# Performance work log

Hardware: AMD Instinct MI355X
Metric: run time of the kernel (lower is better)

## Reference

```python
import jax, jax.numpy as jnp
import numpy as np

N = 200000   # nodes
E = 3200000  # edges
G = 8192     # graphs
F_IN = 28    # one-hot node feature dim (dataset.num_node_features)
D = 50       # embed_dim
H = 16       # hidden_channels
C = 2        # num_classes


def setup_inputs() -> dict:
    key = jax.random.key(0)
    ks = jax.random.split(key, 12)
    x = jax.random.normal(ks[0], (N, F_IN), jnp.float32)
    row = jax.random.randint(ks[1], (E,), 0, N)   # source nodes (edge_index[0])
    col = jax.random.randint(ks[2], (E,), 0, N)   # target nodes (edge_index[1])
    edge_attr = jax.random.uniform(ks[3], (E,), jnp.float32)
    batch = jnp.sort(jax.random.randint(ks[4], (N,), 0, G))
    emb = jax.random.normal(ks[5], (F_IN, D), jnp.float32) * 0.1
    W1 = jax.random.normal(ks[6], (D, H), jnp.float32) * (1.0 / np.sqrt(D))
    b1 = jnp.zeros((H,), jnp.float32)
    W2 = jax.random.normal(ks[7], (H, H), jnp.float32) * (1.0 / np.sqrt(H))
    b2 = jnp.zeros((H,), jnp.float32)
    W3 = jax.random.normal(ks[8], (H, C), jnp.float32) * (1.0 / np.sqrt(H))
    b3 = jnp.zeros((C,), jnp.float32)
    return dict(x=x, row=row, col=col, edge_attr=edge_attr, batch=batch,
                emb=emb, W1=W1, b1=b1, W2=W2, b2=b2, W3=W3, b3=b3)


def gcn_conv(h, row, col, ew, W, b):
    """PyG GCNConv with normalize=True, add_self_loops=True (fill_value=1)."""
    # degree at target nodes, including self-loop weight 1
    deg = jax.ops.segment_sum(ew, col, num_segments=N) + 1.0
    dinv = jnp.where(deg > 0, deg ** -0.5, 0.0)
    hw = h @ W                                   # [N, out]
    norm = dinv[row] * ew * dinv[col]            # [E]
    agg = jax.ops.segment_sum(hw[row] * norm[:, None], col, num_segments=N)
    agg = agg + hw * (dinv * dinv)[:, None]      # self-loop contribution
    return agg + b


def reference(x, row, col, edge_attr, batch, emb, W1, b1, W2, b2, W3, b3):
    # x is one-hot-ish -> argmax -> embedding lookup
    h = emb[jnp.argmax(x, axis=1)]               # [N, D]
    h = jax.nn.relu(gcn_conv(h, row, col, edge_attr, W1, b1))
    # dropout is identity in eval mode
    h = jax.nn.relu(gcn_conv(h, row, col, edge_attr, W2, b2))
    h = gcn_conv(h, row, col, edge_attr, W3, b3)  # [N, C]
    # global mean pool over graphs
    sums = jax.ops.segment_sum(h, batch, num_segments=G)
    cnts = jax.ops.segment_sum(jnp.ones((N,), h.dtype), batch, num_segments=G)
    pooled = sums / jnp.maximum(cnts, 1.0)[:, None]  # [G, C]
    return jax.nn.softmax(pooled, axis=1)
```

## Files before the change

kernel.cpp:

```cpp
#include <hip/hip_runtime.h>
#include <hip/hip_fp16.h>

constexpr int Nn  = 200000;
constexpr int Ne  = 3200000;
constexpr int Ng  = 8192;
constexpr int FIN = 28;
constexpr int DE  = 50;
constexpr int HD  = 16;
constexpr int CD  = 2;

constexpr int NBIN   = (Nn + 255) >> 8;
constexpr int NBLK   = 256;
constexpr int CH     = (Ne + NBLK - 1) / NBLK;
constexpr int CSTR   = 800;
constexpr int LDSCAP = 4608;

__device__ __forceinline__ float dec_ea(unsigned u) {
  return ((float)(u & 16383u) + 0.5f) * (1.0f / 16384.0f);
}

static inline int nblocks(long long n, int bs = 256, int cap = 16384) {
  long long b = (n + bs - 1) / bs;
  return (int)(b < cap ? b : cap);
}

__global__ void k_zero(float* __restrict__ p, int n) {
  int i = blockIdx.x * blockDim.x + threadIdx.x;
  if (i < n) p[i] = 0.0f;
}

__global__ __launch_bounds__(256) void k_count(const int* __restrict__ col,
                                               int* __restrict__ counts) {
  __shared__ int c[NBIN];
  for (int i = threadIdx.x; i < NBIN; i += 256) c[i] = 0;
  __syncthreads();
  int lo = blockIdx.x * CH, hi = min(lo + CH, Ne);
  for (int e = lo + threadIdx.x; e < hi; e += 256) atomicAdd(&c[col[e] >> 8], 1);
  __syncthreads();
  for (int i = threadIdx.x; i < NBIN; i += 256) counts[blockIdx.x * CSTR + i] = c[i];
}

__global__ __launch_bounds__(256) void k_scan1b(int* __restrict__ counts,
                                                int* __restrict__ colTotal) {
  __shared__ int s[256];
  int bin = blockIdx.x, t = threadIdx.x;
  int v = counts[t * CSTR + bin];
  s[t] = v;
  __syncthreads();
  for (int d = 1; d < 256; d <<= 1) {
    int x = (t >= d) ? s[t - d] : 0;
    __syncthreads();
    s[t] += x;
    __syncthreads();
  }
  counts[t * CSTR + bin] = s[t] - v;
  if (t == 255) colTotal[bin] = s[t];
}

__global__ __launch_bounds__(1024) void k_scanBins(const int* __restrict__ colTotal,
                                                   int* __restrict__ binBase,
                                                   int* __restrict__ start) {
  __shared__ int s[1024];
  int t = threadIdx.x;
  int v = (t < NBIN) ? colTotal[t] : 0;
  s[t] = v;
  __syncthreads();
  for (int d = 1; d < 1024; d <<= 1) {
    int x = (t >= d) ? s[t - d] : 0;
    __syncthreads();
    s[t] += x;
    __syncthreads();
  }
  if (t < NBIN) binBase[t] = s[t] - v;
  if (t == NBIN - 1) { binBase[NBIN] = s[t]; start[Nn] = s[t]; }
}

__global__ __launch_bounds__(256) void k_place(const int* __restrict__ row,
                                               const int* __restrict__ col,
                                               const float* __restrict__ ea,
                                               const int* __restrict__ counts,
                                               const int* __restrict__ binBase,
                                               unsigned long long* __restrict__ staged) {
  __shared__ int base[NBIN];
  __shared__ int cur[NBIN];
  for (int i = threadIdx.x; i < NBIN; i += 256) {
    base[i] = binBase[i] + counts[blockIdx.x * CSTR + i];
    cur[i] = 0;
  }
  __syncthreads();
  int lo = blockIdx.x * CH, hi = min(lo + CH, Ne);
  for (int e = lo + threadIdx.x; e < hi; e += 256) {
    int c = col[e], bin = c >> 8;
    unsigned q = (unsigned)__float2int_rd(ea[e] * 16384.0f);
    if (q > 16383u) q = 16383u;
    unsigned lo32 = ((unsigned)row[e] << 14) | q;
    int off = atomicAdd(&cur[bin], 1);
    staged[base[bin] + off] = ((unsigned long long)(unsigned)c << 32) | lo32;
  }
}

__global__ __launch_bounds__(256) void k_fine(const int* __restrict__ binBase,
                                              const unsigned long long* __restrict__ staged,
                                              unsigned* __restrict__ csr,
                                              int* __restrict__ start,
                                              float* __restrict__ dinv) {
  __shared__ int ncnt[256];
  __shared__ int noff[256];
  __shared__ int ncur[256];
  __shared__ float sdeg[256];
  __shared__ unsigned outb[LDSCAP];
  int b = blockIdx.x, t = threadIdx.x;
  int lo = binBase[b];
  int cnt = binBase[b + 1] - lo;
  if (cnt > LDSCAP) cnt = LDSCAP;
  ncnt[t] = 0; ncur[t] = 0; sdeg[t] = 0.0f;
  __syncthreads();
  for (int i = t; i < cnt; i += 256) {
    unsigned long long p = staged[lo + i];
    int cl = (int)((p >> 32) & 255u);
    atomicAdd(&ncnt[cl], 1);
    atomicAdd(&sdeg[cl], dec_ea((unsigned)p));
  }
  __syncthreads();
  int v = ncnt[t];
  noff[t] = v;
  __syncthreads();
  for (int d = 1; d < 256; d <<= 1) {
    int x = (t >= d) ? noff[t - d] : 0;
    __syncthreads();
    noff[t] += x;
    __syncthreads();
  }
  int excl = noff[t] - v;
  __syncthreads();
  noff[t] = excl;
  __syncthreads();
  for (int i = t; i < cnt; i += 256) {
    unsigned long long p = staged[lo + i];
    int cl = (int)((p >> 32) & 255u);
    int idx = noff[cl] + atomicAdd(&ncur[cl], 1);
    outb[idx] = (unsigned)p;
  }
  __syncthreads();
  for (int i = t; i < cnt; i += 256) csr[lo + i] = outb[i];
  int node = (b << 8) + t;
  if (node < Nn) {
    start[node] = lo + noff[t];
    dinv[node] = rsqrtf(sdeg[t] + 1.0f);
  }
}

__global__ void k_embw(const float* __restrict__ emb, const float* __restrict__ W1,
                       float* __restrict__ EW1) {
  int t = threadIdx.x;
  if (t < FIN * HD) {
    int i = t / HD, k = t % HD;
    float s = 0.0f;
    for (int j = 0; j < DE; ++j) s += emb[i * DE + j] * W1[j * HD + k];
    EW1[t] = s;
  }
}

__global__ void k_embed(const float* __restrict__ x, const float* __restrict__ EW1,
                        const float* __restrict__ dinv, __half* __restrict__ hws, int n) {
  int stride = gridDim.x * blockDim.x;
  for (int i = blockIdx.x * blockDim.x + threadIdx.x; i < n; i += stride) {
    const float* xp = x + (long long)i * FIN;
    int arg = 0; float best = xp[0];
#pragma unroll
    for (int j = 1; j < FIN; ++j) { float v = xp[j]; if (v > best) { best = v; arg = j; } }
    float di = dinv[i];
    const float* ep = EW1 + arg * HD;
#pragma unroll
    for (int k = 0; k < HD; ++k) hws[((size_t)i << 4) + k] = __float2half(ep[k] * di);
  }
}

template <int OUTC>
__global__ __launch_bounds__(256) void k_conv(const int* __restrict__ start,
                                              const unsigned* __restrict__ csr,
                                              const __half* __restrict__ hws,
                                              const float* __restrict__ dinv,
                                              const float* __restrict__ bias,
                                              const float* __restrict__ Wn,
                                              __half* __restrict__ outw) {
  int n = blockIdx.x * 4 + (threadIdx.x >> 6);
  if (n >= Nn) return;
  int lane = threadIdx.x & 63;
  int slot = lane >> 3;
  int p    = lane & 7;
  const __half2* h2 = (const __half2*)hws;
  int lo = start[n], hi = start[n + 1];
  float ax = 0.0f, ay = 0.0f;
  for (int j = lo + slot; j < hi; j += 8) {
    unsigned u = csr[j];
    int r = u >> 14;
    float w = dec_ea(u);
    float2 v = __half22float2(h2[(r << 3) + p]);
    ax = fmaf(v.x, w, ax);
    ay = fmaf(v.y, w, ay);
  }
#pragma unroll
  for (int d = 8; d < 64; d <<= 1) {
    ax += __shfl_xor(ax, d, 64);
    ay += __shfl_xor(ay, d, 64);
  }
  float di = dinv[n];
  float2 self = __half22float2(h2[(n << 3) + p]);
  float h0 = fmaxf(di * (ax + self.x) + bias[2 * p + 0], 0.0f);
  float h1 = fmaxf(di * (ay + self.y) + bias[2 * p + 1], 0.0f);
  int k = lane & 15;
  float acc2 = 0.0f;
#pragma unroll
  for (int q = 0; q < 8; ++q) {
    float hj0 = __shfl(h0, q, 64);
    float hj1 = __shfl(h1, q, 64);
    acc2 = fmaf(hj0, Wn[(2 * q + 0) * OUTC + (OUTC == 16 ? k : (k & 1))], acc2);
    acc2 = fmaf(hj1, Wn[(2 * q + 1) * OUTC + (OUTC == 16 ? k : (k & 1))], acc2);
  }
  acc2 *= di;
  if (OUTC == 16) {
    if (lane < 16) outw[((size_t)n << 4) + k] = __float2half(acc2);
  } else {
    if (lane < CD) outw[(size_t)n * CD + k] = __float2half(acc2);
  }
}

__global__ __launch_bounds__(256) void k_conv3pool(const int* __restrict__ start,
                                                   const unsigned* __restrict__ csr,
                                                   const __half* __restrict__ h3,
                                                   const float* __restrict__ dinv,
                                                   const float* __restrict__ b3,
                                                   const int* __restrict__ batch,
                                                   float* __restrict__ sums,
                                                   float* __restrict__ cnts) {
  int wid = threadIdx.x >> 6;
  int lane = threadIdx.x & 63;
  int nsub = lane >> 2;
  int slot = lane & 3;
  int n = (blockIdx.x * 4 + wid) * 16 + nsub;
  if (n >= Nn) return;
  const __half2* h2 = (const __half2*)h3;
  int lo = start[n], hi = start[n + 1];
  float ax = 0.0f, ay = 0.0f;
  for (int j = lo + slot; j < hi; j += 4) {
    unsigned u = csr[j];
    int r = u >> 14;
    float w = dec_ea(u);
    float2 v = __half22float2(h2[r]);
    ax = fmaf(v.x, w, ax);
    ay = fmaf(v.y, w, ay);
  }
  ax += __shfl_xor(ax, 1, 64); ay += __shfl_xor(ay, 1, 64);
  ax += __shfl_xor(ax, 2, 64); ay += __shfl_xor(ay, 2, 64);
  if (slot == 0) {
    float di = dinv[n];
    float2 self = __half22float2(h2[n]);
    float a0 = di * (ax + self.x) + b3[0];
    float a1 = di * (ay + self.y) + b3[1];
    int g = batch[n];
    atomicAdd(&sums[2 * g + 0], a0);
    atomicAdd(&sums[2 * g + 1], a1);
    atomicAdd(&cnts[g], 1.0f);
  }
}

__global__ void k_softmax(const float* __restrict__ sums, const float* __restrict__ cnts,
                          float* __restrict__ out, int g) {
  int stride = gridDim.x * blockDim.x;
  for (int i = blockIdx.x * blockDim.x + threadIdx.x; i < g; i += stride) {
    float cnt = fmaxf(cnts[i], 1.0f);
    float c0 = sums[i * 2 + 0] / cnt;
    float c1 = sums[i * 2 + 1] / cnt;
    float m = fmaxf(c0, c1);
    float e0 = __expf(c0 - m), e1 = __expf(c1 - m);
    float inv = 1.0f / (e0 + e1);
    out[i * 2 + 0] = e0 * inv;
    out[i * 2 + 1] = e1 * inv;
  }
}

extern "C" void kernel_launch(void* const* d_in, const int* in_sizes, int n_in,
                              void* d_out, int out_size, void* d_ws, size_t ws_size,
                              hipStream_t stream) {
  const float* x   = (const float*)d_in[0];
  const int*   row = (const int*)d_in[1];
  const int*   col = (const int*)d_in[2];
  const float* ea  = (const float*)d_in[3];
  const int*   bat = (const int*)d_in[4];
  const float* emb = (const float*)d_in[5];
  const float* W1  = (const float*)d_in[6];
  const float* b1  = (const float*)d_in[7];
  const float* W2  = (const float*)d_in[8];
  const float* b2  = (const float*)d_in[9];
  const float* W3  = (const float*)d_in[10];
  const float* b3  = (const float*)d_in[11];
  float* out = (float*)d_out;

  float* ws = (float*)d_ws;
  size_t o = 0;
  float* sums    = ws + o; o += (size_t)Ng * CD;
  float* cnts    = ws + o; o += Ng;
  float* dinv    = ws + o; o += Nn;
  float* EW1     = ws + o; o += FIN * HD + 16;
  int*   counts  = (int*)(ws + o); o += (size_t)NBLK * CSTR;
  int*   colTot  = (int*)(ws + o); o += CSTR;
  int*   binBase = (int*)(ws + o); o += 1024;
  int*   startp  = (int*)(ws + o); o += Nn + 16;
  unsigned long long* staged = (unsigned long long*)(ws + o); o += (size_t)Ne * 2;
  unsigned* csr  = (unsigned*)(ws + o); o += (size_t)Ne;
  __half* hws1   = (__half*)(ws + o); o += (size_t)Nn * HD / 2;
  __half* hws2   = (__half*)(ws + o); o += (size_t)Nn * HD / 2;
  __half* hw3s   = (__half*)(ws + o); o += (size_t)Nn * CD / 2;
  (void)ws_size; (void)n_in; (void)in_sizes; (void)out_size;

  const int BS = 256;

  k_zero<<<nblocks(Ng * (CD + 1)), BS, 0, stream>>>(sums, Ng * (CD + 1));
  k_embw<<<1, 512, 0, stream>>>(emb, W1, EW1);

  k_count<<<NBLK, 256, 0, stream>>>(col, counts);
  k_scan1b<<<NBIN, 256, 0, stream>>>(counts, colTot);
  k_scanBins<<<1, 1024, 0, stream>>>(colTot, binBase, startp);
  k_place<<<NBLK, 256, 0, stream>>>(row, col, ea, counts, binBase, staged);
  k_fine<<<NBIN, 256, 0, stream>>>(binBase, staged, csr, startp, dinv);

  k_embed<<<nblocks(Nn), BS, 0, stream>>>(x, EW1, dinv, hws1, Nn);

  k_conv<16><<<(Nn + 3) / 4, 256, 0, stream>>>(startp, csr, hws1, dinv, b1, W2, hws2);
  k_conv<2><<<(Nn + 3) / 4, 256, 0, stream>>>(startp, csr, hws2, dinv, b2, W3, hw3s);

  k_conv3pool<<<(Nn + 63) / 64, 256, 0, stream>>>(startp, csr, hw3s, dinv, b3, bat, sums, cnts);

  k_softmax<<<nblocks(Ng), BS, 0, stream>>>(sums, cnts, out, Ng);
}
```

Baseline: 444.7 us.

## Use 8-bit feature storage, LDS-staged edge placement, and fuse embedding into CSR build

Hidden features for the first two convolutions are now stored as 8-bit values (the top byte of an fp16, rounded), halving gather traffic in the neighbour aggregation loops. The placement kernel now uses 512 blocks and first sorts each chunk by bin in LDS, so its global writes are grouped by bin. The embedding/argmax step is fused into the fine CSR kernel, removing one launch and a dinv reread. CSR reads in the conv kernels use nontemporal loads. The 8-bit format has only about 3 mantissa bits, which risks accuracy tolerance failures, and the larger LDS staging buffer may reduce occupancy of the placement kernel.

```diff
diff --git a/kernel.cpp b/kernel.cpp
--- a/kernel.cpp
+++ b/kernel.cpp
@@ -10,13 +10,23 @@
 constexpr int CD  = 2;
 
 constexpr int NBIN   = (Nn + 255) >> 8;
-constexpr int NBLK   = 256;
-constexpr int CH     = (Ne + NBLK - 1) / NBLK;
+constexpr int NBLK   = 512;
+constexpr int CH     = Ne / NBLK;
 constexpr int CSTR   = 800;
 constexpr int LDSCAP = 4608;
 
 __device__ __forceinline__ float dec_ea(unsigned u) {
   return ((float)(u & 16383u) + 0.5f) * (1.0f / 16384.0f);
+}
+
+__device__ __forceinline__ float2 dec8(unsigned short u) {
+  __half lo = __ushort_as_half((unsigned short)((u & 0x00ffu) << 8));
+  __half hi = __ushort_as_half((unsigned short)(u & 0xff00u));
+  return make_float2(__half2float(lo), __half2float(hi));
+}
+__device__ __forceinline__ unsigned char enc8(float f) {
+  unsigned short b = __half_as_ushort(__float2half(f));
+  return (unsigned char)((unsigned short)(b + 0x0080u) >> 8);
 }
 
 static inline int nblocks(long long n, int bs = 256, int cap = 16384) {
@@ -34,27 +44,27 @@
   __shared__ int c[NBIN];
   for (int i = threadIdx.x; i < NBIN; i += 256) c[i] = 0;
   __syncthreads();
-  int lo = blockIdx.x * CH, hi = min(lo + CH, Ne);
-  for (int e = lo + threadIdx.x; e < hi; e += 256) atomicAdd(&c[col[e] >> 8], 1);
+  int lo = blockIdx.x * CH;
+  for (int i = threadIdx.x; i < CH; i += 256) atomicAdd(&c[col[lo + i] >> 8], 1);
   __syncthreads();
   for (int i = threadIdx.x; i < NBIN; i += 256) counts[blockIdx.x * CSTR + i] = c[i];
 }
 
-__global__ __launch_bounds__(256) void k_scan1b(int* __restrict__ counts,
+__global__ __launch_bounds__(512) void k_scan1b(int* __restrict__ counts,
                                                 int* __restrict__ colTotal) {
-  __shared__ int s[256];
+  __shared__ int s[NBLK];
   int bin = blockIdx.x, t = threadIdx.x;
   int v = counts[t * CSTR + bin];
   s[t] = v;
   __syncthreads();
-  for (int d = 1; d < 256; d <<= 1) {
+  for (int d = 1; d < NBLK; d <<= 1) {
     int x = (t >= d) ? s[t - d] : 0;
     __syncthreads();
     s[t] += x;
     __syncthreads();
   }
   counts[t * CSTR + bin] = s[t] - v;
-  if (t == 255) colTotal[bin] = s[t];
+  if (t == NBLK - 1) colTotal[bin] = s[t];
 }
 
 __global__ __launch_bounds__(1024) void k_scanBins(const int* __restrict__ colTotal,
@@ -81,29 +91,74 @@
                                                const int* __restrict__ counts,
                                                const int* __restrict__ binBase,
                                                unsigned long long* __restrict__ staged) {
-  __shared__ int base[NBIN];
-  __shared__ int cur[NBIN];
-  for (int i = threadIdx.x; i < NBIN; i += 256) {
-    base[i] = binBase[i] + counts[blockIdx.x * CSTR + i];
-    cur[i] = 0;
-  }
-  __syncthreads();
-  int lo = blockIdx.x * CH, hi = min(lo + CH, Ne);
-  for (int e = lo + threadIdx.x; e < hi; e += 256) {
+  __shared__ unsigned long long stage[CH];
+  __shared__ int lhist[NBIN];
+  __shared__ int lcur[NBIN];
+  __shared__ int gbase[NBIN];
+  __shared__ int partial[256];
+  int blk = blockIdx.x, t = threadIdx.x;
+  int lo = blk * CH;
+  for (int i = t; i < NBIN; i += 256) { lhist[i] = 0; lcur[i] = 0; }
+  __syncthreads();
+  for (int i = t; i < CH; i += 256) atomicAdd(&lhist[col[lo + i] >> 8], 1);
+  __syncthreads();
+  constexpr int CPT = (NBIN + 255) / 256;
+  int b0 = t * CPT, s = 0;
+#pragma unroll
+  for (int j = 0; j < CPT; ++j) { int b = b0 + j; if (b < NBIN) s += lhist[b]; }
+  partial[t] = s;
+  __syncthreads();
+  for (int d = 1; d < 256; d <<= 1) {
+    int x = (t >= d) ? partial[t - d] : 0;
+    __syncthreads();
+    partial[t] += x;
+    __syncthreads();
+  }
+  int run = partial[t] - s;
+#pragma unroll
+  for (int j = 0; j < CPT; ++j) {
+    int b = b0 + j;
+    if (b < NBIN) { int c = lhist[b]; lhist[b] = run; run += c; }
+  }
+  for (int i = t; i < NBIN; i += 256) gbase[i] = binBase[i] + counts[blk * CSTR + i];
+  __syncthreads();
+  for (int i = t; i < CH; i += 256) {
+    int e = lo + i;
     int c = col[e], bin = c >> 8;
     unsigned q = (unsigned)__float2int_rd(ea[e] * 16384.0f);
     if (q > 16383u) q = 16383u;
-    unsigned lo32 = ((unsigned)row[e] << 14) | q;
-    int off = atomicAdd(&cur[bin], 1);
-    staged[base[bin] + off] = ((unsigned long long)(unsigned)c << 32) | lo32;
-  }
-}
-
-__global__ __launch_bounds__(256) void k_fine(const int* __restrict__ binBase,
-                                              const unsigned long long* __restrict__ staged,
-                                              unsigned* __restrict__ csr,
-                                              int* __restrict__ start,
-                                              float* __restrict__ dinv) {
+    unsigned long long entry =
+        ((unsigned long long)(unsigned)c << 32) | ((unsigned)row[e] << 14) | q;
+    int pos = lhist[bin] + atomicAdd(&lcur[bin], 1);
+    stage[pos] = entry;
+  }
+  __syncthreads();
+  for (int i = t; i < CH; i += 256) {
+    unsigned long long entry = stage[i];
+    int bin = (int)(entry >> 40);
+    staged[gbase[bin] + (i - lhist[bin])] = entry;
+  }
+}
+
+__global__ void k_embw(const float* __restrict__ emb, const float* __restrict__ W1,
+                       float* __restrict__ EW1) {
+  int t = threadIdx.x;
+  if (t < FIN * HD) {
+    int i = t / HD, k = t % HD;
+    float s = 0.0f;
+    for (int j = 0; j < DE; ++j) s += emb[i * DE + j] * W1[j * HD + k];
+    EW1[t] = s;
+  }
+}
+
+__global__ __launch_bounds__(256) void k_finemb(const int* __restrict__ binBase,
+                                                const unsigned long long* __restrict__ staged,
+                                                const float* __restrict__ x,
+                                                const float* __restrict__ EW1,
+                                                unsigned* __restrict__ csr,
+                                                int* __restrict__ start,
+                                                float* __restrict__ dinv,
+                                                unsigned char* __restrict__ hws1) {
   __shared__ int ncnt[256];
   __shared__ int noff[256];
   __shared__ int ncur[256];
@@ -126,9 +181,9 @@
   noff[t] = v;
   __syncthreads();
   for (int d = 1; d < 256; d <<= 1) {
-    int x = (t >= d) ? noff[t - d] : 0;
-    __syncthreads();
-    noff[t] += x;
+    int xsh = (t >= d) ? noff[t - d] : 0;
+    __syncthreads();
+    noff[t] += xsh;
     __syncthreads();
   }
   int excl = noff[t] - v;
@@ -144,59 +199,39 @@
   __syncthreads();
   for (int i = t; i < cnt; i += 256) csr[lo + i] = outb[i];
   int node = (b << 8) + t;
-  if (node < Nn) {
-    start[node] = lo + noff[t];
-    dinv[node] = rsqrtf(sdeg[t] + 1.0f);
-  }
-}
-
-__global__ void k_embw(const float* __restrict__ emb, const float* __restrict__ W1,
-                       float* __restrict__ EW1) {
-  int t = threadIdx.x;
-  if (t < FIN * HD) {
-    int i = t / HD, k = t % HD;
-    float s = 0.0f;
-    for (int j = 0; j < DE; ++j) s += emb[i * DE + j] * W1[j * HD + k];
-    EW1[t] = s;
-  }
-}
-
-__global__ void k_embed(const float* __restrict__ x, const float* __restrict__ EW1,
-                        const float* __restrict__ dinv, __half* __restrict__ hws, int n) {
-  int stride = gridDim.x * blockDim.x;
-  for (int i = blockIdx.x * blockDim.x + threadIdx.x; i < n; i += stride) {
-    const float* xp = x + (long long)i * FIN;
-    int arg = 0; float best = xp[0];
-#pragma unroll
-    for (int j = 1; j < FIN; ++j) { float v = xp[j]; if (v > best) { best = v; arg = j; } }
-    float di = dinv[i];
-    const float* ep = EW1 + arg * HD;
-#pragma unroll
-    for (int k = 0; k < HD; ++k) hws[((size_t)i << 4) + k] = __float2half(ep[k] * di);
-  }
+  if (node >= Nn) return;
+  start[node] = lo + noff[t];
+  float di = rsqrtf(sdeg[t] + 1.0f);
+  dinv[node] = di;
+  const float* xp = x + (long long)node * FIN;
+  int arg = 0; float best = xp[0];
+#pragma unroll
+  for (int j = 1; j < FIN; ++j) { float vv = xp[j]; if (vv > best) { best = vv; arg = j; } }
+  const float* ep = EW1 + arg * HD;
+#pragma unroll
+  for (int k = 0; k < HD; ++k) hws1[((size_t)node << 4) + k] = enc8(ep[k] * di);
 }
 
 template <int OUTC>
 __global__ __launch_bounds__(256) void k_conv(const int* __restrict__ start,
                                               const unsigned* __restrict__ csr,
-                                              const __half* __restrict__ hws,
+                                              const unsigned short* __restrict__ f8,
                                               const float* __restrict__ dinv,
                                               const float* __restrict__ bias,
                                               const float* __restrict__ Wn,
-                                              __half* __restrict__ outw) {
+                                              void* __restrict__ outw) {
   int n = blockIdx.x * 4 + (threadIdx.x >> 6);
   if (n >= Nn) return;
   int lane = threadIdx.x & 63;
   int slot = lane >> 3;
   int p    = lane & 7;
-  const __half2* h2 = (const __half2*)hws;
   int lo = start[n], hi = start[n + 1];
   float ax = 0.0f, ay = 0.0f;
   for (int j = lo + slot; j < hi; j += 8) {
-    unsigned u = csr[j];
+    unsigned u = __builtin_nontemporal_load(csr + j);
     int r = u >> 14;
     float w = dec_ea(u);
-    float2 v = __half22float2(h2[(r << 3) + p]);
+    float2 v = dec8(f8[(r << 3) + p]);
     ax = fmaf(v.x, w, ax);
     ay = fmaf(v.y, w, ay);
   }
@@ -206,7 +241,7 @@
     ay += __shfl_xor(ay, d, 64);
   }
   float di = dinv[n];
-  float2 self = __half22float2(h2[(n << 3) + p]);
+  float2 self = dec8(f8[(n << 3) + p]);
   float h0 = fmaxf(di * (ax + self.x) + bias[2 * p + 0], 0.0f);
   float h1 = fmaxf(di * (ay + self.y) + bias[2 * p + 1], 0.0f);
   int k = lane & 15;
@@ -220,9 +255,9 @@
   }
   acc2 *= di;
   if (OUTC == 16) {
-    if (lane < 16) outw[((size_t)n << 4) + k] = __float2half(acc2);
+    if (lane < 16) ((unsigned char*)outw)[((size_t)n << 4) + k] = enc8(acc2);
   } else {
-    if (lane < CD) outw[(size_t)n * CD + k] = __float2half(acc2);
+    if (lane < CD) ((__half*)outw)[(size_t)n * CD + k] = __float2half(acc2);
   }
 }
 
@@ -244,7 +279,7 @@
   int lo = start[n], hi = start[n + 1];
   float ax = 0.0f, ay = 0.0f;
   for (int j = lo + slot; j < hi; j += 4) {
-    unsigned u = csr[j];
+    unsigned u = __builtin_nontemporal_load(csr + j);
     int r = u >> 14;
     float w = dec_ea(u);
     float2 v = __half22float2(h2[r]);
@@ -309,8 +344,8 @@
   int*   startp  = (int*)(ws + o); o += Nn + 16;
   unsigned long long* staged = (unsigned long long*)(ws + o); o += (size_t)Ne * 2;
   unsigned* csr  = (unsigned*)(ws + o); o += (size_t)Ne;
-  __half* hws1   = (__half*)(ws + o); o += (size_t)Nn * HD / 2;
-  __half* hws2   = (__half*)(ws + o); o += (size_t)Nn * HD / 2;
+  unsigned char* hws1 = (unsigned char*)(ws + o); o += (size_t)Nn * HD / 4;
+  unsigned char* hws2 = (unsigned char*)(ws + o); o += (size_t)Nn * HD / 4;
   __half* hw3s   = (__half*)(ws + o); o += (size_t)Nn * CD / 2;
   (void)ws_size; (void)n_in; (void)in_sizes; (void)out_size;
 
@@ -320,15 +355,15 @@
   k_embw<<<1, 512, 0, stream>>>(emb, W1, EW1);
 
   k_count<<<NBLK, 256, 0, stream>>>(col, counts);
-  k_scan1b<<<NBIN, 256, 0, stream>>>(counts, colTot);
+  k_scan1b<<<NBIN, NBLK, 0, stream>>>(counts, colTot);
   k_scanBins<<<1, 1024, 0, stream>>>(colTot, binBase, startp);
   k_place<<<NBLK, 256, 0, stream>>>(row, col, ea, counts, binBase, staged);
-  k_fine<<<NBIN, 256, 0, stream>>>(binBase, staged, csr, startp, dinv);
-
-  k_embed<<<nblocks(Nn), BS, 0, stream>>>(x, EW1, dinv, hws1, Nn);
-
-  k_conv<16><<<(Nn + 3) / 4, 256, 0, stream>>>(startp, csr, hws1, dinv, b1, W2, hws2);
-  k_conv<2><<<(Nn + 3) / 4, 256, 0, stream>>>(startp, csr, hws2, dinv, b2, W3, hw3s);
+  k_finemb<<<NBIN, 256, 0, stream>>>(binBase, staged, x, EW1, csr, startp, dinv, hws1);
+
+  k_conv<16><<<(Nn + 3) / 4, 256, 0, stream>>>(startp, csr, (const unsigned short*)hws1,
+                                               dinv, b1, W2, hws2);
+  k_conv<2><<<(Nn + 3) / 4, 256, 0, stream>>>(startp, csr, (const unsigned short*)hws2,
+                                              dinv, b2, W3, hw3s);
 
   k_conv3pool<<<(Nn + 63) / 64, 256, 0, stream>>>(startp, csr, hw3s, dinv, b3, bat, sums, cnts);
 
```

Result: no change. 443.1 us (-0.4%).
